# Kernel optimization log

Measured on AMD Instinct MI355X. Metric: run time of the kernel, lower is better.

## Reference

```python
import jax, jax.numpy as jnp
import numpy as np

# NF4 codebook (bitsandbytes nf4 quant_type), 16 levels in [-1, 1]
NF4 = jnp.array([
    -1.0, -0.6961928009986877, -0.5250730514526367, -0.39491748809814453,
    -0.28444138169288635, -0.18477343022823334, -0.09105003625154495, 0.0,
    0.07958029955625534, 0.16093020141124725, 0.24611230194568634,
    0.33791524171829224, 0.44070982933044434, 0.5626170039176941,
    0.7229568362236023, 1.0], dtype=jnp.float32)
BLOCK = 64  # bitsandbytes default quant block size

TOKENS, HD, M = 8192, 4096, 11008


def dequant_nf4(codes, scales):
    # codes: [out, in] int in [0,16); scales: [out, in//BLOCK] per-block absmax
    out_f, in_f = codes.shape
    w = NF4[codes].reshape(out_f, in_f // BLOCK, BLOCK) * scales[:, :, None]
    return w.reshape(out_f, in_f)


def setup_inputs() -> dict:
    key = jax.random.key(0)
    k = jax.random.split(key, 7)
    return {
        "x": jax.random.normal(k[0], (TOKENS, HD), dtype=jnp.float32),
        "gate_codes": jax.random.randint(k[1], (M, HD), 0, 16, dtype=jnp.int32),
        "gate_scales": jax.random.uniform(k[2], (M, HD // BLOCK), dtype=jnp.float32) * 0.1,
        "up_codes": jax.random.randint(k[3], (M, HD), 0, 16, dtype=jnp.int32),
        "up_scales": jax.random.uniform(k[4], (M, HD // BLOCK), dtype=jnp.float32) * 0.1,
        "down_codes": jax.random.randint(k[5], (HD, M), 0, 16, dtype=jnp.int32),
        "down_scales": jax.random.uniform(k[6], (HD, M // BLOCK), dtype=jnp.float32) * 0.1,
    }


def reference(x, gate_codes, gate_scales, up_codes, up_scales, down_codes, down_scales):
    Wg = dequant_nf4(gate_codes, gate_scales)   # [m, hd]
    Wu = dequant_nf4(up_codes, up_scales)       # [m, hd]
    Wd = dequant_nf4(down_codes, down_scales)   # [hd, m]
    g = jnp.einsum('td,md->tm', x, Wg)          # gate_proj(x)
    u = jnp.einsum('td,md->tm', x, Wu)          # up_proj(x)
    h = jax.nn.silu(g) * u                      # SwiGLU
    return jnp.einsum('tm,dm->td', h, Wd)       # down_proj
```

## Files before the change

### kernel.cpp

```cpp
#include <hip/hip_runtime.h>
#include <hip/hip_bf16.h>

typedef _Float16 half8 __attribute__((ext_vector_type(8)));
typedef float floatx4 __attribute__((ext_vector_type(4)));

__device__ __constant__ float NF4_TAB[16] = {
    -1.0f, -0.6961928009986877f, -0.5250730514526367f, -0.39491748809814453f,
    -0.28444138169288635f, -0.18477343022823334f, -0.09105003625154495f, 0.0f,
    0.07958029955625534f, 0.16093020141124725f, 0.24611230194568634f,
    0.33791524171829224f, 0.44070982933044434f, 0.5626170039176941f,
    0.7229568362236023f, 1.0f};

typedef __attribute__((address_space(3))) void lds_t;
typedef __attribute__((address_space(1))) void gbl_t;

__device__ __forceinline__ void gload16(const void* g, void* l) {
  __builtin_amdgcn_global_load_lds((gbl_t*)g, (lds_t*)l, 16, 0, 0);
}

__global__ void cvt_f32_to_f16(const float* __restrict__ in,
                               _Float16* __restrict__ out, int total8) {
  int stride = gridDim.x * blockDim.x;
  for (int i = blockIdx.x * blockDim.x + threadIdx.x; i < total8; i += stride) {
    long e = (long)i * 8;
    const float4* ip = reinterpret_cast<const float4*>(in + e);
    float4 a = ip[0], b = ip[1];
    half8 o;
    o[0] = (_Float16)a.x; o[1] = (_Float16)a.y;
    o[2] = (_Float16)a.z; o[3] = (_Float16)a.w;
    o[4] = (_Float16)b.x; o[5] = (_Float16)b.y;
    o[6] = (_Float16)b.z; o[7] = (_Float16)b.w;
    *reinterpret_cast<half8*>(out + e) = o;
  }
}

__global__ void dequant_nf4(const int* __restrict__ codes,
                            const float* __restrict__ scales,
                            _Float16* __restrict__ out,
                            int total8, int C, int CB) {
  __shared__ float lut[16];
  if (threadIdx.x < 16) lut[threadIdx.x] = NF4_TAB[threadIdx.x];
  __syncthreads();
  int stride = gridDim.x * blockDim.x;
  for (int i = blockIdx.x * blockDim.x + threadIdx.x; i < total8; i += stride) {
    long e = (long)i * 8;
    int row = (int)(e / C);
    int col = (int)(e - (long)row * C);
    float sc = scales[row * CB + (col >> 6)];
    const int4* cp = reinterpret_cast<const int4*>(codes + e);
    int4 c0 = cp[0];
    int4 c1 = cp[1];
    half8 o;
    o[0] = (_Float16)(lut[c0.x & 15] * sc);
    o[1] = (_Float16)(lut[c0.y & 15] * sc);
    o[2] = (_Float16)(lut[c0.z & 15] * sc);
    o[3] = (_Float16)(lut[c0.w & 15] * sc);
    o[4] = (_Float16)(lut[c1.x & 15] * sc);
    o[5] = (_Float16)(lut[c1.y & 15] * sc);
    o[6] = (_Float16)(lut[c1.z & 15] * sc);
    o[7] = (_Float16)(lut[c1.w & 15] * sc);
    *reinterpret_cast<half8*>(out + e) = o;
  }
}

#define FENCE() asm volatile("" ::: "memory")

template <int K, int N, int EPI>
__global__ __launch_bounds__(512, 2) void gemm256(
    const _Float16* __restrict__ A,
    const _Float16* __restrict__ B,
    _Float16* __restrict__ GH,
    float* __restrict__ OUT) {
  constexpr int NT = K / 64;
  constexpr int NBC = N / 256;
  constexpr int NWG = (8192 / 256) * NBC;
  __shared__ __align__(16) _Float16 lds[2 * 32768];

  const int t = threadIdx.x;
  const int lane = t & 63;
  const int wave = t >> 6;
  const int wm = wave >> 2;
  const int wn = wave & 3;

  int bid = blockIdx.x;
  bid = (bid & 7) * (NWG >> 3) + (bid >> 3);
  const int bm = bid / NBC, bn = bid % NBC;

  const int lc = (t & 3) ^ ((t >> 3) & 3);
  const _Float16* gA = A + ((long)bm * 256 + (t >> 2)) * K + lc * 8;
  const _Float16* gB = B + ((long)bn * 256 + (t >> 2)) * K + lc * 8;
  const long rstep = (long)128 * K;
  const int dst = t * 8;

  const int rA = wm * 128 + (lane & 15);
  const int rB = wn * 64 + (lane & 15);
  const int ckA = ((lane >> 4) ^ ((rA >> 1) & 3)) * 8;
  const int ckB = ((lane >> 4) ^ ((rB >> 1) & 3)) * 8;
  const int offA = rA * 32 + ckA;
  const int offB = 16384 + rB * 32 + ckB;

#define STAGE_SLOT(gp, slab, koff, dbuf)                                   \
  gload16((gp) + (koff), lds + (dbuf) * 32768 + (slab) + dst);             \
  gload16((gp) + (koff) + rstep, lds + (dbuf) * 32768 + (slab) + dst + 4096);

  STAGE_SLOT(gA, 0, 0, 0);
  STAGE_SLOT(gB, 16384, 0, 0);
  STAGE_SLOT(gA, 8192, 32, 0);
  STAGE_SLOT(gB, 24576, 32, 0);
  gA += 64; gB += 64;
  asm volatile("s_waitcnt vmcnt(4)" ::: "memory");
  __builtin_amdgcn_s_barrier();
  FENCE();

  floatx4 acc[8][4] = {};

  for (int kt = 0; kt < NT; ++kt) {
    const int cb = kt & 1;
    const int sbuf = cb ^ 1;
    const _Float16* lb = lds + cb * 32768;
    const bool st = (kt + 1 < NT);
    const bool last = (kt == NT - 1);

    half8 a[8], b[2];

#pragma unroll
    for (int i = 0; i < 8; ++i)
      a[i] = *reinterpret_cast<const half8*>(&lb[offA + i * 512]);
    b[0] = *reinterpret_cast<const half8*>(&lb[offB]);
    b[1] = *reinterpret_cast<const half8*>(&lb[offB + 512]);
    if (st) { STAGE_SLOT(gA, 0, 0, sbuf); }
    __builtin_amdgcn_s_barrier();
    FENCE();
    __builtin_amdgcn_s_setprio(1);
#pragma unroll
    for (int i = 0; i < 8; ++i) {
      acc[i][0] = __builtin_amdgcn_mfma_f32_16x16x32_f16(a[i], b[0], acc[i][0], 0, 0, 0);
      acc[i][1] = __builtin_amdgcn_mfma_f32_16x16x32_f16(a[i], b[1], acc[i][1], 0, 0, 0);
    }
    __builtin_amdgcn_s_setprio(0);
    __builtin_amdgcn_s_barrier();
    FENCE();

    b[0] = *reinterpret_cast<const half8*>(&lb[offB + 2 * 512]);
    b[1] = *reinterpret_cast<const half8*>(&lb[offB + 3 * 512]);
    if (st) { STAGE_SLOT(gB, 16384, 0, sbuf); }
    if (last) { asm volatile("s_waitcnt vmcnt(0)" ::: "memory"); }
    else      { asm volatile("s_waitcnt vmcnt(4)" ::: "memory"); }
    __builtin_amdgcn_s_barrier();
    FENCE();
    __builtin_amdgcn_s_setprio(1);
#pragma unroll
    for (int i = 0; i < 8; ++i) {
      acc[i][2] = __builtin_amdgcn_mfma_f32_16x16x32_f16(a[i], b[0], acc[i][2], 0, 0, 0);
      acc[i][3] = __builtin_amdgcn_mfma_f32_16x16x32_f16(a[i], b[1], acc[i][3], 0, 0, 0);
    }
    __builtin_amdgcn_s_setprio(0);
    __builtin_amdgcn_s_barrier();
    FENCE();

#pragma unroll
    for (int i = 0; i < 8; ++i)
      a[i] = *reinterpret_cast<const half8*>(&lb[8192 + offA + i * 512]);
    b[0] = *reinterpret_cast<const half8*>(&lb[8192 + offB]);
    b[1] = *reinterpret_cast<const half8*>(&lb[8192 + offB + 512]);
    if (st) { STAGE_SLOT(gA, 8192, 32, sbuf); }
    __builtin_amdgcn_s_barrier();
    FENCE();
    __builtin_amdgcn_s_setprio(1);
#pragma unroll
    for (int i = 0; i < 8; ++i) {
      acc[i][0] = __builtin_amdgcn_mfma_f32_16x16x32_f16(a[i], b[0], acc[i][0], 0, 0, 0);
      acc[i][1] = __builtin_amdgcn_mfma_f32_16x16x32_f16(a[i], b[1], acc[i][1], 0, 0, 0);
    }
    __builtin_amdgcn_s_setprio(0);
    __builtin_amdgcn_s_barrier();
    FENCE();

    b[0] = *reinterpret_cast<const half8*>(&lb[8192 + offB + 2 * 512]);
    b[1] = *reinterpret_cast<const half8*>(&lb[8192 + offB + 3 * 512]);
    if (st) { STAGE_SLOT(gB, 24576, 32, sbuf); gA += 64; gB += 64; }
    if (!last) { asm volatile("s_waitcnt vmcnt(4)" ::: "memory"); }
    __builtin_amdgcn_s_barrier();
    FENCE();
    __builtin_amdgcn_s_setprio(1);
#pragma unroll
    for (int i = 0; i < 8; ++i) {
      acc[i][2] = __builtin_amdgcn_mfma_f32_16x16x32_f16(a[i], b[0], acc[i][2], 0, 0, 0);
      acc[i][3] = __builtin_amdgcn_mfma_f32_16x16x32_f16(a[i], b[1], acc[i][3], 0, 0, 0);
    }
    __builtin_amdgcn_s_setprio(0);
    __builtin_amdgcn_s_barrier();
    FENCE();
  }
#undef STAGE_SLOT

  const int r0 = bm * 256 + wm * 128 + (lane >> 4) * 4;
  const int c0 = bn * 256 + wn * 64 + (lane & 15);
#pragma unroll
  for (int i = 0; i < 8; ++i) {
#pragma unroll
    for (int j = 0; j < 4; ++j) {
#pragma unroll
      for (int ii = 0; ii < 4; ++ii) {
        const long idx = (long)(r0 + i * 16 + ii) * N + (c0 + j * 16);
        if (EPI == 0) {
          GH[idx] = (_Float16)acc[i][j][ii];
        } else if (EPI == 1) {
          float u = acc[i][j][ii];
          float g = (float)GH[idx];
          GH[idx] = (_Float16)(g / (1.0f + __expf(-g)) * u);
        } else {
          OUT[idx] = acc[i][j][ii];
        }
      }
    }
  }
}

extern "C" void kernel_launch(void* const* d_in, const int* in_sizes, int n_in,
                              void* d_out, int out_size, void* d_ws, size_t ws_size,
                              hipStream_t stream) {
  const float* x           = (const float*)d_in[0];
  const int*   gate_codes  = (const int*)d_in[1];
  const float* gate_scales = (const float*)d_in[2];
  const int*   up_codes    = (const int*)d_in[3];
  const float* up_scales   = (const float*)d_in[4];
  const int*   down_codes  = (const int*)d_in[5];
  const float* down_scales = (const float*)d_in[6];
  float* out = (float*)d_out;

  const long T = 8192, HD = 4096, M = 11008;

  char* ws = (char*)d_ws;
  _Float16* x16 = (_Float16*)ws;
  _Float16* W   = (_Float16*)(ws + T * HD * 2);
  _Float16* gh  = (_Float16*)(ws + T * HD * 2 + M * HD * 2);

  cvt_f32_to_f16<<<2048, 256, 0, stream>>>(x, x16, (int)(T * HD / 8));

  dequant_nf4<<<2048, 256, 0, stream>>>(gate_codes, gate_scales, W,
                                        (int)(M * HD / 8), (int)HD, (int)(HD / 64));
  gemm256<4096, 11008, 0><<<(8192 / 256) * (11008 / 256), 512, 0, stream>>>(
      x16, W, gh, nullptr);

  dequant_nf4<<<2048, 256, 0, stream>>>(up_codes, up_scales, W,
                                        (int)(M * HD / 8), (int)HD, (int)(HD / 64));
  gemm256<4096, 11008, 1><<<(8192 / 256) * (11008 / 256), 512, 0, stream>>>(
      x16, W, gh, nullptr);

  dequant_nf4<<<2048, 256, 0, stream>>>(down_codes, down_scales, W,
                                        (int)(HD * M / 8), (int)M, (int)(M / 64));
  gemm256<11008, 4096, 2><<<(8192 / 256) * (4096 / 256), 512, 0, stream>>>(
      gh, W, nullptr, out);
}
```

Before: 2.304 ms.

## Fuse NF4 dequantization into GEMM B-tile staging with packed 4-bit weights

Replaces the standalone dequant kernels, which wrote full fp16 weight matrices, with a pre-pass that packs int32 codes into 4-bit nibbles in a k-tile-major layout and transposes the scales. The GEMM then loads the packed nibbles and the scale per k-tile and dequantizes in registers with byte-permute table lookups, writing fp16 into swizzled LDS. This cuts the weight traffic each GEMM reads from global memory. In exchange the main loop does ALU dequant work, fully drains vmcnt/lgkmcnt every iteration, and applies the scale in fp16 rather than fp32.

```diff
diff --git a/kernel.cpp b/kernel.cpp
--- a/kernel.cpp
+++ b/kernel.cpp
@@ -2,20 +2,65 @@
 #include <hip/hip_bf16.h>
 
 typedef _Float16 half8 __attribute__((ext_vector_type(8)));
+typedef _Float16 h2 __attribute__((ext_vector_type(2)));
 typedef float floatx4 __attribute__((ext_vector_type(4)));
-
-__device__ __constant__ float NF4_TAB[16] = {
-    -1.0f, -0.6961928009986877f, -0.5250730514526367f, -0.39491748809814453f,
-    -0.28444138169288635f, -0.18477343022823334f, -0.09105003625154495f, 0.0f,
-    0.07958029955625534f, 0.16093020141124725f, 0.24611230194568634f,
-    0.33791524171829224f, 0.44070982933044434f, 0.5626170039176941f,
-    0.7229568362236023f, 1.0f};
+typedef unsigned int uint;
 
 typedef __attribute__((address_space(3))) void lds_t;
 typedef __attribute__((address_space(1))) void gbl_t;
 
 __device__ __forceinline__ void gload16(const void* g, void* l) {
   __builtin_amdgcn_global_load_lds((gbl_t*)g, (lds_t*)l, 16, 0, 0);
+}
+
+#define FENCE() asm volatile("" ::: "memory")
+
+#if __has_builtin(__builtin_amdgcn_perm)
+#define PERM(a, b, s) __builtin_amdgcn_perm((a), (b), (s))
+#else
+__device__ __forceinline__ uint PERM(uint a, uint b, uint s) {
+  unsigned long long comb = ((unsigned long long)a << 32) | b;
+  uint r = 0;
+#pragma unroll
+  for (int i = 0; i < 4; ++i) {
+    uint idx = (s >> (8 * i)) & 0xFF;
+    uint by = (idx < 8) ? (uint)((comb >> (8 * idx)) & 0xFF) : 0u;
+    r |= by << (8 * i);
+  }
+  return r;
+}
+#endif
+
+#define TL0 0x52339200u
+#define TL1 0x00D4EA8Du
+#define TL2 0x68E02618u
+#define TL3 0x00C9800Du
+#define TH0 0xB6B8B9BCu
+#define TH1 0x00ADB1B4u
+#define TH2 0x3533312Du
+#define TH3 0x3C393837u
+
+__device__ __forceinline__ void deq4(uint s, uint sc2, uint& r0, uint& r1) {
+  uint s7 = s & 0x07070707u;
+  uint m = s & 0x08080808u;
+  uint m8 = (m << 5) - (m >> 3);
+  uint lo = (PERM(TL3, TL2, s7) & m8) | (PERM(TL1, TL0, s) & ~m8);
+  uint hi = (PERM(TH3, TH2, s7) & m8) | (PERM(TH1, TH0, s) & ~m8);
+  uint a0 = PERM(hi, lo, 0x05010400u);
+  uint a1 = PERM(hi, lo, 0x07030602u);
+  h2 v0 = __builtin_bit_cast(h2, a0) * __builtin_bit_cast(h2, sc2);
+  h2 v1 = __builtin_bit_cast(h2, a1) * __builtin_bit_cast(h2, sc2);
+  r0 = __builtin_bit_cast(uint, v0);
+  r1 = __builtin_bit_cast(uint, v1);
+}
+
+__device__ __forceinline__ void deq8(uint d, uint sc2, uint* o) {
+  uint e = d & 0x0F0F0F0Fu;
+  uint od = (d >> 4) & 0x0F0F0F0Fu;
+  uint sA = PERM(od, e, 0x05010400u);
+  uint sB = PERM(od, e, 0x07030602u);
+  deq4(sA, sc2, o[0], o[1]);
+  deq4(sB, sc2, o[2], o[3]);
 }
 
 __global__ void cvt_f32_to_f16(const float* __restrict__ in,
@@ -34,41 +79,48 @@
   }
 }
 
-__global__ void dequant_nf4(const int* __restrict__ codes,
-                            const float* __restrict__ scales,
-                            _Float16* __restrict__ out,
-                            int total8, int C, int CB) {
-  __shared__ float lut[16];
-  if (threadIdx.x < 16) lut[threadIdx.x] = NF4_TAB[threadIdx.x];
-  __syncthreads();
-  int stride = gridDim.x * blockDim.x;
-  for (int i = blockIdx.x * blockDim.x + threadIdx.x; i < total8; i += stride) {
-    long e = (long)i * 8;
-    int row = (int)(e / C);
-    int col = (int)(e - (long)row * C);
-    float sc = scales[row * CB + (col >> 6)];
-    const int4* cp = reinterpret_cast<const int4*>(codes + e);
-    int4 c0 = cp[0];
-    int4 c1 = cp[1];
-    half8 o;
-    o[0] = (_Float16)(lut[c0.x & 15] * sc);
-    o[1] = (_Float16)(lut[c0.y & 15] * sc);
-    o[2] = (_Float16)(lut[c0.z & 15] * sc);
-    o[3] = (_Float16)(lut[c0.w & 15] * sc);
-    o[4] = (_Float16)(lut[c1.x & 15] * sc);
-    o[5] = (_Float16)(lut[c1.y & 15] * sc);
-    o[6] = (_Float16)(lut[c1.z & 15] * sc);
-    o[7] = (_Float16)(lut[c1.w & 15] * sc);
-    *reinterpret_cast<half8*>(out + e) = o;
-  }
-}
-
-#define FENCE() asm volatile("" ::: "memory")
+__global__ void pack_nf4(const int* __restrict__ codes,
+                         unsigned char* __restrict__ pk, int R, int C) {
+  const int CT = C >> 4;
+  const long total = (long)R * CT;
+  const long stride = (long)gridDim.x * blockDim.x;
+  for (long i = blockIdx.x * blockDim.x + threadIdx.x; i < total; i += stride) {
+    int r = (int)(i / CT);
+    int g = (int)(i - (long)r * CT);
+    int c0 = g << 4;
+    const int4* p = reinterpret_cast<const int4*>(codes + (long)r * C + c0);
+    int4 a = p[0], b = p[1], c = p[2], d = p[3];
+    uint w0 = (uint)(a.x & 15) | ((uint)(a.y & 15) << 4) |
+              ((uint)(a.z & 15) << 8) | ((uint)(a.w & 15) << 12) |
+              ((uint)(b.x & 15) << 16) | ((uint)(b.y & 15) << 20) |
+              ((uint)(b.z & 15) << 24) | ((uint)(b.w & 15) << 28);
+    uint w1 = (uint)(c.x & 15) | ((uint)(c.y & 15) << 4) |
+              ((uint)(c.z & 15) << 8) | ((uint)(c.w & 15) << 12) |
+              ((uint)(d.x & 15) << 16) | ((uint)(d.y & 15) << 20) |
+              ((uint)(d.z & 15) << 24) | ((uint)(d.w & 15) << 28);
+    int kt = c0 >> 6;
+    long off = ((long)kt * R + r) * 32 + ((c0 & 63) >> 1);
+    uint2 v; v.x = w0; v.y = w1;
+    *reinterpret_cast<uint2*>(pk + off) = v;
+  }
+}
+
+__global__ void pack_scales(const float* __restrict__ s,
+                            float* __restrict__ o, int R, int CB) {
+  const long total = (long)R * CB;
+  const long stride = (long)gridDim.x * blockDim.x;
+  for (long i = blockIdx.x * blockDim.x + threadIdx.x; i < total; i += stride) {
+    int r = (int)(i / CB);
+    int cb = (int)(i - (long)r * CB);
+    o[(long)cb * R + r] = s[i];
+  }
+}
 
 template <int K, int N, int EPI>
 __global__ __launch_bounds__(512, 2) void gemm256(
     const _Float16* __restrict__ A,
-    const _Float16* __restrict__ B,
+    const unsigned char* __restrict__ BPK,
+    const float* __restrict__ BSC,
     _Float16* __restrict__ GH,
     float* __restrict__ OUT) {
   constexpr int NT = K / 64;
@@ -88,9 +140,15 @@
 
   const int lc = (t & 3) ^ ((t >> 3) & 3);
   const _Float16* gA = A + ((long)bm * 256 + (t >> 2)) * K + lc * 8;
-  const _Float16* gB = B + ((long)bn * 256 + (t >> 2)) * K + lc * 8;
   const long rstep = (long)128 * K;
   const int dst = t * 8;
+
+  const int brow = t >> 1;
+  const int bhalf = t & 1;
+  const unsigned char* gPK = BPK + ((long)(bn * 256 + brow)) * 32 + bhalf * 16;
+  const float* gSC = BSC + (bn * 256 + brow);
+  const int wh = (brow >> 1) & 3;
+  _Float16* wbase0 = (_Float16*)lds + 16384 + bhalf * 8192 + brow * 32;
 
   const int rA = wm * 128 + (lane & 15);
   const int rB = wn * 64 + (lane & 15);
@@ -99,16 +157,36 @@
   const int offA = rA * 32 + ckA;
   const int offB = 16384 + rB * 32 + ckB;
 
-#define STAGE_SLOT(gp, slab, koff, dbuf)                                   \
-  gload16((gp) + (koff), lds + (dbuf) * 32768 + (slab) + dst);             \
-  gload16((gp) + (koff) + rstep, lds + (dbuf) * 32768 + (slab) + dst + 4096);
-
-  STAGE_SLOT(gA, 0, 0, 0);
-  STAGE_SLOT(gB, 16384, 0, 0);
-  STAGE_SLOT(gA, 8192, 32, 0);
-  STAGE_SLOT(gB, 24576, 32, 0);
-  gA += 64; gB += 64;
-  asm volatile("s_waitcnt vmcnt(4)" ::: "memory");
+  uint4 pkv;
+  float scv;
+
+  auto stage_b = [&](int db) {
+    _Float16 sh = (_Float16)scv;
+    unsigned short us = __builtin_bit_cast(unsigned short, sh);
+    uint sc2 = (uint)us * 0x10001u;
+    uint w0[4], w1[4], w2[4], w3[4];
+    deq8(pkv.x, sc2, w0);
+    deq8(pkv.y, sc2, w1);
+    deq8(pkv.z, sc2, w2);
+    deq8(pkv.w, sc2, w3);
+    _Float16* wb = wbase0 + db * 32768;
+    *reinterpret_cast<uint4*>(wb + (0 ^ wh) * 8) = *reinterpret_cast<uint4*>(w0);
+    *reinterpret_cast<uint4*>(wb + (1 ^ wh) * 8) = *reinterpret_cast<uint4*>(w1);
+    *reinterpret_cast<uint4*>(wb + (2 ^ wh) * 8) = *reinterpret_cast<uint4*>(w2);
+    *reinterpret_cast<uint4*>(wb + (3 ^ wh) * 8) = *reinterpret_cast<uint4*>(w3);
+  };
+
+  gload16(gA, (_Float16*)lds + dst);
+  gload16(gA + rstep, (_Float16*)lds + dst + 4096);
+  gload16(gA + 32, (_Float16*)lds + 8192 + dst);
+  gload16(gA + 32 + rstep, (_Float16*)lds + 8192 + dst + 4096);
+  FENCE();
+  pkv = *reinterpret_cast<const uint4*>(gPK);
+  scv = *gSC;
+  gA += 64;
+  asm volatile("s_waitcnt vmcnt(0)" ::: "memory");
+  stage_b(0);
+  asm volatile("s_waitcnt lgkmcnt(0)" ::: "memory");
   __builtin_amdgcn_s_barrier();
   FENCE();
 
@@ -117,9 +195,9 @@
   for (int kt = 0; kt < NT; ++kt) {
     const int cb = kt & 1;
     const int sbuf = cb ^ 1;
-    const _Float16* lb = lds + cb * 32768;
+    const _Float16* lb = (_Float16*)lds + cb * 32768;
+    _Float16* sb = (_Float16*)lds + sbuf * 32768;
     const bool st = (kt + 1 < NT);
-    const bool last = (kt == NT - 1);
 
     half8 a[8], b[2];
 
@@ -128,7 +206,16 @@
       a[i] = *reinterpret_cast<const half8*>(&lb[offA + i * 512]);
     b[0] = *reinterpret_cast<const half8*>(&lb[offB]);
     b[1] = *reinterpret_cast<const half8*>(&lb[offB + 512]);
-    if (st) { STAGE_SLOT(gA, 0, 0, sbuf); }
+    if (st) {
+      gload16(gA, sb + dst);
+      gload16(gA + rstep, sb + dst + 4096);
+      gload16(gA + 32, sb + 8192 + dst);
+      gload16(gA + 32 + rstep, sb + 8192 + dst + 4096);
+      FENCE();
+      pkv = *reinterpret_cast<const uint4*>(gPK + (long)(kt + 1) * ((long)N * 32));
+      scv = gSC[(long)(kt + 1) * N];
+      gA += 64;
+    }
     __builtin_amdgcn_s_barrier();
     FENCE();
     __builtin_amdgcn_s_setprio(1);
@@ -143,9 +230,6 @@
 
     b[0] = *reinterpret_cast<const half8*>(&lb[offB + 2 * 512]);
     b[1] = *reinterpret_cast<const half8*>(&lb[offB + 3 * 512]);
-    if (st) { STAGE_SLOT(gB, 16384, 0, sbuf); }
-    if (last) { asm volatile("s_waitcnt vmcnt(0)" ::: "memory"); }
-    else      { asm volatile("s_waitcnt vmcnt(4)" ::: "memory"); }
     __builtin_amdgcn_s_barrier();
     FENCE();
     __builtin_amdgcn_s_setprio(1);
@@ -163,7 +247,7 @@
       a[i] = *reinterpret_cast<const half8*>(&lb[8192 + offA + i * 512]);
     b[0] = *reinterpret_cast<const half8*>(&lb[8192 + offB]);
     b[1] = *reinterpret_cast<const half8*>(&lb[8192 + offB + 512]);
-    if (st) { STAGE_SLOT(gA, 8192, 32, sbuf); }
+    if (st) { stage_b(sbuf); }
     __builtin_amdgcn_s_barrier();
     FENCE();
     __builtin_amdgcn_s_setprio(1);
@@ -178,8 +262,6 @@
 
     b[0] = *reinterpret_cast<const half8*>(&lb[8192 + offB + 2 * 512]);
     b[1] = *reinterpret_cast<const half8*>(&lb[8192 + offB + 3 * 512]);
-    if (st) { STAGE_SLOT(gB, 24576, 32, sbuf); gA += 64; gB += 64; }
-    if (!last) { asm volatile("s_waitcnt vmcnt(4)" ::: "memory"); }
     __builtin_amdgcn_s_barrier();
     FENCE();
     __builtin_amdgcn_s_setprio(1);
@@ -189,10 +271,10 @@
       acc[i][3] = __builtin_amdgcn_mfma_f32_16x16x32_f16(a[i], b[1], acc[i][3], 0, 0, 0);
     }
     __builtin_amdgcn_s_setprio(0);
-    __builtin_amdgcn_s_barrier();
-    FENCE();
-  }
-#undef STAGE_SLOT
+    asm volatile("s_waitcnt vmcnt(0) lgkmcnt(0)" ::: "memory");
+    __builtin_amdgcn_s_barrier();
+    FENCE();
+  }
 
   const int r0 = bm * 256 + wm * 128 + (lane >> 4) * 4;
   const int c0 = bn * 256 + wn * 64 + (lane & 15);
@@ -232,24 +314,27 @@
   const long T = 8192, HD = 4096, M = 11008;
 
   char* ws = (char*)d_ws;
-  _Float16* x16 = (_Float16*)ws;
-  _Float16* W   = (_Float16*)(ws + T * HD * 2);
-  _Float16* gh  = (_Float16*)(ws + T * HD * 2 + M * HD * 2);
+  _Float16* x16 = (_Float16*)ws;                     ws += T * HD * 2;
+  _Float16* gh  = (_Float16*)ws;                     ws += T * M * 2;
+  unsigned char* pkG = (unsigned char*)ws;           ws += M * HD / 2;
+  unsigned char* pkU = (unsigned char*)ws;           ws += M * HD / 2;
+  unsigned char* pkD = (unsigned char*)ws;           ws += HD * M / 2;
+  float* scG = (float*)ws;                           ws += (HD / 64) * M * 4;
+  float* scU = (float*)ws;                           ws += (HD / 64) * M * 4;
+  float* scD = (float*)ws;
 
   cvt_f32_to_f16<<<2048, 256, 0, stream>>>(x, x16, (int)(T * HD / 8));
-
-  dequant_nf4<<<2048, 256, 0, stream>>>(gate_codes, gate_scales, W,
-                                        (int)(M * HD / 8), (int)HD, (int)(HD / 64));
+  pack_nf4<<<2048, 256, 0, stream>>>(gate_codes, pkG, (int)M, (int)HD);
+  pack_nf4<<<2048, 256, 0, stream>>>(up_codes, pkU, (int)M, (int)HD);
+  pack_nf4<<<2048, 256, 0, stream>>>(down_codes, pkD, (int)HD, (int)M);
+  pack_scales<<<2048, 256, 0, stream>>>(gate_scales, scG, (int)M, (int)(HD / 64));
+  pack_scales<<<2048, 256, 0, stream>>>(up_scales, scU, (int)M, (int)(HD / 64));
+  pack_scales<<<2048, 256, 0, stream>>>(down_scales, scD, (int)HD, (int)(M / 64));
+
   gemm256<4096, 11008, 0><<<(8192 / 256) * (11008 / 256), 512, 0, stream>>>(
-      x16, W, gh, nullptr);
-
-  dequant_nf4<<<2048, 256, 0, stream>>>(up_codes, up_scales, W,
-                                        (int)(M * HD / 8), (int)HD, (int)(HD / 64));
+      x16, pkG, scG, gh, nullptr);
   gemm256<4096, 11008, 1><<<(8192 / 256) * (11008 / 256), 512, 0, stream>>>(
-      x16, W, gh, nullptr);
-
-  dequant_nf4<<<2048, 256, 0, stream>>>(down_codes, down_scales, W,
-                                        (int)(HD * M / 8), (int)M, (int)(M / 64));
+      x16, pkU, scU, gh, nullptr);
   gemm256<11008, 4096, 2><<<(8192 / 256) * (4096 / 256), 512, 0, stream>>>(
-      gh, W, nullptr, out);
-}
+      gh, pkD, scD, nullptr, out);
+}
```

New measurement: 2.791 ms. 1.21x slower.
